# Optimization experiments

Measured on AMD Instinct MI355X. Metric: run time of the kernel, lower is better.

## Reference

```python
import jax, jax.numpy as jnp
import numpy as np

# ---- constants matching the torch module / entmax normmax_bisect defaults ----
ALPHA = 5.0                 # normmax alpha (entmax normmax_bisect default)
N_BISECT = 50               # bisection iterations
K_EXP = 1.0 / (ALPHA - 1.0)        # p_i propto (z_i - tau)_+^{1/(alpha-1)}
AK_EXP = ALPHA / (ALPHA - 1.0)     # norm condition: sum (z-tau)_+^{alpha/(alpha-1)} = 1
EPS = 1e-8                  # module epsilon
LN_EPS = 1e-5               # torch LayerNorm default eps

B, N, C, D = 32, 1024, 64, 768


def _bisect_tau(z):
    # z: [..., S]; find tau with f(tau) = sum_i relu(z_i - tau)^AK_EXP - 1 = 0 (f decreasing)
    max_val = jnp.max(z, axis=-1, keepdims=True)
    lo, hi = max_val - 1.0, max_val  # f(lo) >= 0, f(hi) = -1 < 0

    def body(_, carry):
        lo, hi = carry
        tau = 0.5 * (lo + hi)
        f = jnp.sum(jnp.maximum(z - tau, 0.0) ** AK_EXP, axis=-1, keepdims=True) - 1.0
        lo = jnp.where(f >= 0, tau, lo)
        hi = jnp.where(f >= 0, hi, tau)
        return (lo, hi)

    lo, hi = jax.lax.fori_loop(0, N_BISECT, body, (lo, hi))
    return 0.5 * (lo + hi)


def normmax_last(z):
    # normmax over last axis: p = s / sum(s), s = relu(z - tau)^{1/(alpha-1)}, ||s||_alpha = 1
    tau = _bisect_tau(z)
    u = jnp.maximum(z - tau, 0.0)
    u_safe = jnp.where(u > 0, u, 1.0)
    s = jnp.where(u > 0, u_safe ** K_EXP, 0.0)
    return s / jnp.sum(s, axis=-1, keepdims=True)


def layernorm(x, scale, bias):
    mu = jnp.mean(x, axis=-1, keepdims=True)
    var = jnp.mean((x - mu) ** 2, axis=-1, keepdims=True)
    return (x - mu) * jax.lax.rsqrt(var + LN_EPS) * scale + bias


def setup_inputs() -> dict:
    key = jax.random.key(0)
    ks = jax.random.split(key, 10)
    w = lambda k, shp: (jax.random.normal(k, shp, dtype=jnp.float32) * 0.02)
    return {
        "features": jax.random.normal(ks[0], (B, N, D), dtype=jnp.float32),
        "slots_init": jax.random.normal(ks[1], (B, C, D), dtype=jnp.float32),
        "mask": jax.random.randint(ks[2], (B, N), 0, 2, dtype=jnp.int32),
        "ln_f_scale": jnp.ones((D,), jnp.float32),
        "ln_f_bias": jnp.zeros((D,), jnp.float32),
        "ln_s_scale": jnp.ones((D,), jnp.float32),
        "ln_s_bias": jnp.zeros((D,), jnp.float32),
        "Wk": w(ks[3], (D, D)),
        "Wv": w(ks[4], (D, D)),
        "Wq": w(ks[5], (D, D)),
        "W_ih": w(ks[6], (3 * D, D)),
        "W_hh": w(ks[7], (3 * D, D)),
        "b_ih": jnp.zeros((3 * D,), jnp.float32),
        "b_hh": jnp.zeros((3 * D,), jnp.float32),
    }


def reference(features, slots_init, mask, ln_f_scale, ln_f_bias, ln_s_scale, ln_s_bias,
              Wk, Wv, Wq, W_ih, W_hh, b_ih, b_hh):
    f = layernorm(features, ln_f_scale, ln_f_bias)        # [B,N,D]
    k = f @ Wk.T
    v = f @ Wv.T
    b, n, d = v.shape
    c = slots_init.shape[1]
    m = mask[:, None, :] != 0                             # [B,1,N], broadcasts over C

    # num_iterations = 1; straight-through (detach trick) is the identity here.
    slots_prev = slots_init
    s = layernorm(slots_init, ln_s_scale, ln_s_bias)
    q = s @ Wq.T                                          # [B,C,D]
    logits = jnp.einsum('bcd,bnd->bcn', q, k) * (1.0 / np.sqrt(d))
    logits = jnp.where(m, logits, 0.0)                    # masked_fill(mask==0, 0)
    # normmax over the slot axis (dim=1)
    attn = jnp.moveaxis(normmax_last(jnp.moveaxis(logits, 1, -1)), -1, 1)  # [B,C,N]
    attn = jnp.where(m, attn, 0.0)
    attn_wm = attn / (jnp.sum(attn, axis=-1, keepdims=True) + EPS)
    updates = jnp.einsum('bcn,bnd->bcd', attn_wm, v)      # [B,C,D]

    # torch GRUCell: r,z,n gate order
    x = updates.reshape(-1, d)
    h = slots_prev.reshape(-1, d)
    gi = x @ W_ih.T + b_ih
    gh = h @ W_hh.T + b_hh
    ir, iz, in_ = jnp.split(gi, 3, axis=-1)
    hr, hz, hn = jnp.split(gh, 3, axis=-1)
    r = jax.nn.sigmoid(ir + hr)
    zg = jax.nn.sigmoid(iz + hz)
    ng = jnp.tanh(in_ + r * hn)
    h_new = (1.0 - zg) * ng + zg * h
    slots = h_new.reshape(b, c, d)
    return slots, attn
```

## Files before the change

### kernel.cpp

```cpp
#include <hip/hip_runtime.h>
#include <cstdint>
#include <cmath>

#define DEVINL __device__ __forceinline__


using f32x4  = __attribute__((ext_vector_type(4))) float;
using bf16x8 = __attribute__((ext_vector_type(8))) __bf16;
using u16x8  = __attribute__((ext_vector_type(8))) unsigned short;
using u16x4  = __attribute__((ext_vector_type(4))) unsigned short;
using fl4    = __attribute__((ext_vector_type(4))) float;

DEVINL float bf2f(unsigned short h) {
    unsigned int u = ((unsigned int)h) << 16;
    float f; __builtin_memcpy(&f, &u, 4); return f;
}
DEVINL unsigned short f2bf(float f) {
    unsigned int u; __builtin_memcpy(&u, &f, 4);
    u += 0x7FFFu + ((u >> 16) & 1u);
    return (unsigned short)(u >> 16);
}
DEVINL float sqrt_raw(float x) {
    float r; asm("v_sqrt_f32 %0, %1" : "=v"(r) : "v"(x)); return r;
}

DEVINL void gload_lds16(const unsigned short* g, unsigned short* l) {
    __builtin_amdgcn_global_load_lds(
        (__attribute__((address_space(1))) void*)g,
        (__attribute__((address_space(3))) void*)l,
        16, 0, 0);
}

__global__ __launch_bounds__(256)
void tr2_f2b_split(const float* __restrict__ Wq, const float* __restrict__ Wk,
                   unsigned short* __restrict__ WqT_i, unsigned short* __restrict__ WkT_i)
{
    constexpr int S = 768 * 768;
    const int o = blockIdx.x * 256 + threadIdx.x;
    if (o >= 2 * S) return;
    const float* x; unsigned short* y; int i;
    if (o < S) { x = Wq; y = WqT_i; i = o; }
    else       { x = Wk; y = WkT_i; i = o - S; }
    const int e = i / 768, d = i - e * 768;
    const float v = x[d * 768 + e];
    const unsigned short h = f2bf(v);
    y[(long)e * 1536 + d]       = h;
    y[(long)e * 1536 + 768 + d] = f2bf(v - bf2f(h));
}

__global__ __launch_bounds__(256)
void conv2_fused(const float* __restrict__ Wih, const float* __restrict__ Whh,
                 const float* __restrict__ sl,  const float* __restrict__ Wv,
                 unsigned short* __restrict__ Wihb, unsigned short* __restrict__ Whhb,
                 unsigned short* __restrict__ slb,  unsigned short* __restrict__ Wvb)
{
    constexpr int S1 = 3 * 768 * 768;
    constexpr int S2 = S1 + 3 * 768 * 768;
    constexpr int S3 = S2 + 32 * 64 * 768;
    constexpr int S4 = S3 + 768 * 768;
    const int i = (blockIdx.x * 256 + threadIdx.x) * 4;
    if (i >= S4) return;
    const float* src; unsigned short* dst; int off;
    if (i < S1)      { src = Wih; dst = Wihb; off = i; }
    else if (i < S2) { src = Whh; dst = Whhb; off = i - S1; }
    else if (i < S3) { src = sl;  dst = slb;  off = i - S2; }
    else             { src = Wv;  dst = Wvb;  off = i - S3; }
    fl4 v = *(const fl4*)(src + off);
    u16x4 o;
#pragma unroll
    for (int j = 0; j < 4; ++j) o[j] = f2bf(v[j]);
    *(u16x4*)(dst + off) = o;
}

template<int BM, int BN, int WAVES_M, int WAVES_N, int OUTMODE>
__global__ __launch_bounds__(256)
void gemm_bt3(const unsigned short* __restrict__ AB, const unsigned short* __restrict__ BB,
              void* __restrict__ out1,
              int N, int K, long sA, long sB, long sC, float alpha)
{
    constexpr int BK = 32;
    constexpr int WM = BM / WAVES_M, WN = BN / WAVES_N;
    constexpr int MT = WM / 16, NT = WN / 16;
    __shared__ alignas(16) unsigned short Ash[BM * BK], Asl[BM * BK];
    __shared__ alignas(16) unsigned short Bsh[BN * BK], Bsl[BN * BK];

    const int bz = blockIdx.z;
    AB += (long)bz * sA;
    BB += (long)bz * sB;
    const int row0 = blockIdx.y * BM, col0 = blockIdx.x * BN;
    const int tid = threadIdx.x, l = tid & 63, w = tid >> 6;
    const int wm = w / WAVES_N, wn = w % WAVES_N;
    const int fr = l & 15, fq = l >> 4;

    f32x4 acc[MT][NT] = {};
    constexpr int ACALLS = (BM * BK) / (256 * 8);
    constexpr int BCALLS = (BN * BK) / (256 * 8);

    for (int kt = 0; kt < K; kt += BK) {
#pragma unroll
        for (int c = 0; c < ACALLS; ++c) {
            const int e = (c * 256 + tid) * 8;
            const long rb = (long)(row0 + (e >> 5)) * (2 * K) + kt + (e & 31);
            gload_lds16(AB + rb, &Ash[e]);
            gload_lds16(AB + rb + K, &Asl[e]);
        }
#pragma unroll
        for (int c = 0; c < BCALLS; ++c) {
            const int e = (c * 256 + tid) * 8;
            const long rb = (long)(col0 + (e >> 5)) * (2 * K) + kt + (e & 31);
            gload_lds16(BB + rb, &Bsh[e]);
            gload_lds16(BB + rb + K, &Bsl[e]);
        }
        __syncthreads();

        bf16x8 afh[MT], afl[MT], bfh[NT], bfl[NT];
#pragma unroll
        for (int m = 0; m < MT; ++m) {
            const int o = (wm * WM + m * 16 + fr) * BK + fq * 8;
            afh[m] = __builtin_bit_cast(bf16x8, *(const u16x8*)&Ash[o]);
            afl[m] = __builtin_bit_cast(bf16x8, *(const u16x8*)&Asl[o]);
        }
#pragma unroll
        for (int n = 0; n < NT; ++n) {
            const int o = (wn * WN + n * 16 + fr) * BK + fq * 8;
            bfh[n] = __builtin_bit_cast(bf16x8, *(const u16x8*)&Bsh[o]);
            bfl[n] = __builtin_bit_cast(bf16x8, *(const u16x8*)&Bsl[o]);
        }
#pragma unroll
        for (int m = 0; m < MT; ++m)
#pragma unroll
            for (int n = 0; n < NT; ++n) {
                acc[m][n] = __builtin_amdgcn_mfma_f32_16x16x32_bf16(afh[m], bfh[n], acc[m][n], 0, 0, 0);
                acc[m][n] = __builtin_amdgcn_mfma_f32_16x16x32_bf16(afh[m], bfl[n], acc[m][n], 0, 0, 0);
                acc[m][n] = __builtin_amdgcn_mfma_f32_16x16x32_bf16(afl[m], bfh[n], acc[m][n], 0, 0, 0);
            }
        __syncthreads();
    }

#pragma unroll
    for (int m = 0; m < MT; ++m) {
        const int gr = row0 + wm * WM + m * 16 + fq * 4;
#pragma unroll
        for (int n = 0; n < NT; ++n) {
            const int gc = col0 + wn * WN + n * 16 + fr;
#pragma unroll
            for (int j = 0; j < 4; ++j) {
                const float v = acc[m][n][j] * alpha;
                if (OUTMODE == 0) {
                    ((float*)out1)[(long)bz * sC + (long)(gr + j) * N + gc] = v;
                } else {
                    unsigned short* ob = (unsigned short*)out1;
                    const long rb = (long)(gr + j) * (2 * N) + gc;
                    const unsigned short h = f2bf(v);
                    ob[rb] = h;
                    ob[rb + N] = f2bf(v - bf2f(h));
                }
            }
        }
    }
}

template<int BM, int BN, int WAVES_M, int WAVES_N, bool OUT_F32>
__global__ __launch_bounds__(256)
void gemm_bt(const unsigned short* __restrict__ A,
             const unsigned short* __restrict__ B,
             void* __restrict__ Cv,
             int N, int K, long sA, long sB, long sC, float alpha)
{
    constexpr int BK = 32;
    constexpr int WM = BM / WAVES_M, WN = BN / WAVES_N;
    constexpr int MT = WM / 16, NT = WN / 16;
    __shared__ alignas(16) unsigned short As[BM * BK];
    __shared__ alignas(16) unsigned short Bs[BN * BK];

    const int bz = blockIdx.z;
    A += (long)bz * sA;
    B += (long)bz * sB;
    const int row0 = blockIdx.y * BM, col0 = blockIdx.x * BN;
    const int tid = threadIdx.x, l = tid & 63, w = tid >> 6;
    const int wm = w / WAVES_N, wn = w % WAVES_N;
    const int fr = l & 15, fq = l >> 4;

    f32x4 acc[MT][NT] = {};
    constexpr int ACALLS = (BM * BK) / (256 * 8);
    constexpr int BCALLS = (BN * BK) / (256 * 8);

    for (int kt = 0; kt < K; kt += BK) {
#pragma unroll
        for (int c = 0; c < ACALLS; ++c) {
            const int e = (c * 256 + tid) * 8;
            gload_lds16(A + (long)(row0 + (e >> 5)) * K + kt + (e & 31), &As[e]);
        }
#pragma unroll
        for (int c = 0; c < BCALLS; ++c) {
            const int e = (c * 256 + tid) * 8;
            gload_lds16(B + (long)(col0 + (e >> 5)) * K + kt + (e & 31), &Bs[e]);
        }
        __syncthreads();

        bf16x8 af[MT], bfr[NT];
#pragma unroll
        for (int m = 0; m < MT; ++m)
            af[m] = __builtin_bit_cast(bf16x8, *(const u16x8*)&As[(wm * WM + m * 16 + fr) * BK + fq * 8]);
#pragma unroll
        for (int n = 0; n < NT; ++n)
            bfr[n] = __builtin_bit_cast(bf16x8, *(const u16x8*)&Bs[(wn * WN + n * 16 + fr) * BK + fq * 8]);
#pragma unroll
        for (int m = 0; m < MT; ++m)
#pragma unroll
            for (int n = 0; n < NT; ++n)
                acc[m][n] = __builtin_amdgcn_mfma_f32_16x16x32_bf16(af[m], bfr[n], acc[m][n], 0, 0, 0);
        __syncthreads();
    }

#pragma unroll
    for (int m = 0; m < MT; ++m) {
        const int gr = row0 + wm * WM + m * 16 + fq * 4;
#pragma unroll
        for (int n = 0; n < NT; ++n) {
            const int gc = col0 + wn * WN + n * 16 + fr;
#pragma unroll
            for (int j = 0; j < 4; ++j) {
                const float v = acc[m][n][j] * alpha;
                if (OUT_F32) ((float*)Cv)[(long)bz * sC + (long)(gr + j) * N + gc] = v;
                else ((unsigned short*)Cv)[(long)bz * sC + (long)(gr + j) * N + gc] = f2bf(v);
            }
        }
    }
}

template<int BM, int BN, int WAVES_M, int WAVES_N>
__global__ __launch_bounds__(256)
void gemm_nt_rs(const unsigned short* __restrict__ A,
                const unsigned short* __restrict__ Bm,
                unsigned short* __restrict__ C,
                int N, int K, long sA, long sB, long sC)
{
    constexpr int BK = 32;
    constexpr int WM = BM / WAVES_M, WN = BN / WAVES_N;
    constexpr int MT = WM / 16, NT = WN / 16;
    __shared__ alignas(16) unsigned short As[BM * BK];
    __shared__ alignas(16) unsigned short Bs[BN * BK];
    __shared__ float rsums[BM];

    const int bz = blockIdx.z;
    A += (long)bz * sA;
    Bm += (long)bz * sB;
    const int row0 = blockIdx.y * BM, col0 = blockIdx.x * BN;
    const int tid = threadIdx.x, l = tid & 63, w = tid >> 6;
    const int wm = w / WAVES_N, wn = w % WAVES_N;
    const int fr = l & 15, fq = l >> 4;

    f32x4 acc[MT][NT] = {};
    float rsum = 0.f;
    constexpr int ACALLS = (BM * BK) / (256 * 8);
    constexpr int TPR = BN / 8;
    constexpr int RPP = 256 / TPR;
    const int br = tid / TPR, bc8 = (tid % TPR) * 8;

    for (int kt = 0; kt < K; kt += BK) {
#pragma unroll
        for (int c = 0; c < ACALLS; ++c) {
            const int e = (c * 256 + tid) * 8;
            gload_lds16(A + (long)(row0 + (e >> 5)) * K + kt + (e & 31), &As[e]);
        }
#pragma unroll
        for (int p = 0; p < BK / RPP; ++p) {
            const int r = p * RPP + br;
            u16x8 vv = *(const u16x8*)(Bm + (long)(kt + r) * (2 * N) + col0 + bc8);
#pragma unroll
            for (int j = 0; j < 8; ++j) Bs[(bc8 + j) * BK + r] = vv[j];
        }
        __syncthreads();

        if (tid < BM) {
#pragma unroll
            for (int kk = 0; kk < BK / 8; ++kk) {
                u16x8 vv = *(const u16x8*)&As[tid * BK + kk * 8];
#pragma unroll
                for (int j = 0; j < 8; ++j) rsum += bf2f(vv[j]);
            }
        }

        bf16x8 af[MT], bfr[NT];
#pragma unroll
        for (int m = 0; m < MT; ++m)
            af[m] = __builtin_bit_cast(bf16x8, *(const u16x8*)&As[(wm * WM + m * 16 + fr) * BK + fq * 8]);
#pragma unroll
        for (int n = 0; n < NT; ++n)
            bfr[n] = __builtin_bit_cast(bf16x8, *(const u16x8*)&Bs[(wn * WN + n * 16 + fr) * BK + fq * 8]);
#pragma unroll
        for (int m = 0; m < MT; ++m)
#pragma unroll
            for (int n = 0; n < NT; ++n)
                acc[m][n] = __builtin_amdgcn_mfma_f32_16x16x32_bf16(af[m], bfr[n], acc[m][n], 0, 0, 0);
        __syncthreads();
    }

    if (tid < BM) rsums[tid] = rsum;
    __syncthreads();

#pragma unroll
    for (int m = 0; m < MT; ++m) {
        const int lr = wm * WM + m * 16 + fq * 4;
        const int gr = row0 + lr;
#pragma unroll
        for (int n = 0; n < NT; ++n) {
            const int gc = col0 + wn * WN + n * 16 + fr;
#pragma unroll
            for (int j = 0; j < 4; ++j) {
                const float inv = 1.f / (rsums[lr + j] + 1e-8f);
                C[(long)bz * sC + (long)(gr + j) * N + gc] = f2bf(acc[m][n][j] * inv);
            }
        }
    }
}

__global__ __launch_bounds__(256)
void ln_fused(const float* __restrict__ xf, const float* __restrict__ gf,
              const float* __restrict__ bf,
              unsigned short* __restrict__ fi,
              const float* __restrict__ xs, const float* __restrict__ gs,
              const float* __restrict__ bs,
              unsigned short* __restrict__ si,
              int nrows_f)
{
    constexpr int D = 768;
    const int lane = threadIdx.x & 63;
    long row = (long)blockIdx.x * 4 + (threadIdx.x >> 6);
    const float *x, *g, *bb_;
    unsigned short* y;
    if (row < nrows_f) { x = xf; g = gf; bb_ = bf; y = fi; }
    else { row -= nrows_f; x = xs; g = gs; bb_ = bs; y = si; }

    const float* xr = x + row * D;
    const int eA = lane * 8;
    const int eB = 512 + lane * 8;
    float v[16];
    {
        fl4 a = *(const fl4*)(xr + eA);
        fl4 b = *(const fl4*)(xr + eA + 4);
#pragma unroll
        for (int j = 0; j < 4; ++j) { v[j] = a[j]; v[4 + j] = b[j]; }
    }
    if (lane < 32) {
        fl4 a = *(const fl4*)(xr + eB);
        fl4 b = *(const fl4*)(xr + eB + 4);
#pragma unroll
        for (int j = 0; j < 4; ++j) { v[8 + j] = a[j]; v[12 + j] = b[j]; }
    }
    float s = 0.f, s2 = 0.f;
#pragma unroll
    for (int j = 0; j < 8; ++j) { s += v[j]; s2 += v[j] * v[j]; }
    if (lane < 32) {
#pragma unroll
        for (int j = 8; j < 16; ++j) { s += v[j]; s2 += v[j] * v[j]; }
    }
#pragma unroll
    for (int o = 1; o < 64; o <<= 1) { s += __shfl_xor(s, o); s2 += __shfl_xor(s2, o); }
    const float mu  = s / (float)D;
    const float var = s2 / (float)D - mu * mu;
    const float r   = rsqrtf(var + 1e-5f);

    unsigned short* yr = y + row * (2 * D);
    {
        fl4 g0 = *(const fl4*)(g + eA), g1 = *(const fl4*)(g + eA + 4);
        fl4 b0 = *(const fl4*)(bb_ + eA), b1 = *(const fl4*)(bb_ + eA + 4);
        u16x8 oh, ol;
#pragma unroll
        for (int j = 0; j < 8; ++j) {
            const float gg = (j < 4) ? g0[j] : g1[j - 4];
            const float be = (j < 4) ? b0[j] : b1[j - 4];
            const float yv = (v[j] - mu) * r * gg + be;
            oh[j] = f2bf(yv);
            ol[j] = f2bf(yv - bf2f(oh[j]));
        }
        *(u16x8*)(yr + eA) = oh;
        *(u16x8*)(yr + D + eA) = ol;
    }
    if (lane < 32) {
        fl4 g0 = *(const fl4*)(g + eB), g1 = *(const fl4*)(g + eB + 4);
        fl4 b0 = *(const fl4*)(bb_ + eB), b1 = *(const fl4*)(bb_ + eB + 4);
        u16x8 oh, ol;
#pragma unroll
        for (int j = 0; j < 8; ++j) {
            const float gg = (j < 4) ? g0[j] : g1[j - 4];
            const float be = (j < 4) ? b0[j] : b1[j - 4];
            const float yv = (v[8 + j] - mu) * r * gg + be;
            oh[j] = f2bf(yv);
            ol[j] = f2bf(yv - bf2f(oh[j]));
        }
        *(u16x8*)(yr + eB) = oh;
        *(u16x8*)(yr + D + eB) = ol;
    }
}

__global__ __launch_bounds__(256)
void normmax_cols(const float* __restrict__ logits, const int* __restrict__ mask,
                  float* __restrict__ attn_f32, unsigned short* __restrict__ attn_b16)
{
    constexpr int N = 1024, C = 64;
    const int b = blockIdx.y;
    const int tid = threadIdx.x, l = tid & 63, w = tid >> 6;
    const int n = blockIdx.x * 64 + w * 16 + (l & 15);
    const int cb = (l >> 4) * 16;
    const long base = (long)b * C * N + n;
    const float* Lb = logits + base;
    const int m = mask[b * N + n];

    float z[16];
#pragma unroll
    for (int i = 0; i < 16; ++i) z[i] = m ? Lb[(cb + i) * N] : 0.f;

    float mx = z[0];
#pragma unroll
    for (int i = 1; i < 16; ++i) mx = fmaxf(mx, z[i]);
    mx = fmaxf(mx, __shfl_xor(mx, 16));
    mx = fmaxf(mx, __shfl_xor(mx, 32));

    float lo = mx - 1.f, hi = mx;
    for (int it = 0; it < 34; ++it) {
        const float tau = 0.5f * (lo + hi);
        float f = 0.f;
#pragma unroll
        for (int i = 0; i < 16; ++i) {
            const float u = fmaxf(z[i] - tau, 0.f);
            f += u * sqrt_raw(sqrt_raw(u));
        }
        f += __shfl_xor(f, 16);
        f += __shfl_xor(f, 32);
        if (f >= 1.f) lo = tau; else hi = tau;
    }
    const float tau = 0.5f * (lo + hi);
    float sv[16]; float ss = 0.f;
#pragma unroll
    for (int i = 0; i < 16; ++i) {
        const float u = fmaxf(z[i] - tau, 0.f);
        sv[i] = sqrt_raw(sqrt_raw(u));
        ss += sv[i];
    }
    ss += __shfl_xor(ss, 16);
    ss += __shfl_xor(ss, 32);
    const float inv = 1.f / ss;
#pragma unroll
    for (int i = 0; i < 16; ++i) {
        const float a = m ? sv[i] * inv : 0.f;
        attn_f32[base + (long)(cb + i) * N] = a;
        attn_b16[base + (long)(cb + i) * N] = f2bf(a);
    }
}

__global__ __launch_bounds__(256)
void gru_gates(const float* __restrict__ gi, const float* __restrict__ gh,
               const float* __restrict__ b_ih, const float* __restrict__ b_hh,
               const float* __restrict__ h, float* __restrict__ out)
{
    constexpr int D = 768;
    const int t = blockIdx.x * 256 + threadIdx.x;
    const int row = t / (D / 4), d = (t - row * (D / 4)) * 4;
    const float* gir = gi + (long)row * 3 * D;
    const float* ghr = gh + (long)row * 3 * D;
    fl4 ir  = *(const fl4*)(gir + d);
    fl4 iz  = *(const fl4*)(gir + D + d);
    fl4 in_ = *(const fl4*)(gir + 2 * D + d);
    fl4 hr  = *(const fl4*)(ghr + d);
    fl4 hz  = *(const fl4*)(ghr + D + d);
    fl4 hn  = *(const fl4*)(ghr + 2 * D + d);
    fl4 bir = *(const fl4*)(b_ih + d);
    fl4 biz = *(const fl4*)(b_ih + D + d);
    fl4 bin = *(const fl4*)(b_ih + 2 * D + d);
    fl4 bhr = *(const fl4*)(b_hh + d);
    fl4 bhz = *(const fl4*)(b_hh + D + d);
    fl4 bhn = *(const fl4*)(b_hh + 2 * D + d);
    fl4 hv  = *(const fl4*)(h + (long)row * D + d);
    fl4 o;
#pragma unroll
    for (int j = 0; j < 4; ++j) {
        const float r  = 1.f / (1.f + expf(-(ir[j] + bir[j] + hr[j] + bhr[j])));
        const float zg = 1.f / (1.f + expf(-(iz[j] + biz[j] + hz[j] + bhz[j])));
        const float ng = tanhf(in_[j] + bin[j] + r * (hn[j] + bhn[j]));
        o[j] = (1.f - zg) * ng + zg * hv[j];
    }
    *(fl4*)(out + (long)row * D + d) = o;
}

extern "C" void kernel_launch(void* const* d_in, const int* in_sizes, int n_in,
                              void* d_out, int out_size, void* d_ws, size_t ws_size,
                              hipStream_t stream)
{
    const float* features = (const float*)d_in[0];
    const float* slots    = (const float*)d_in[1];
    const int*   mask     = (const int*)d_in[2];
    const float* lnf_g = (const float*)d_in[3];
    const float* lnf_b = (const float*)d_in[4];
    const float* lns_g = (const float*)d_in[5];
    const float* lns_b = (const float*)d_in[6];
    const float* Wk  = (const float*)d_in[7];
    const float* Wv  = (const float*)d_in[8];
    const float* Wq  = (const float*)d_in[9];
    const float* Wih = (const float*)d_in[10];
    const float* Whh = (const float*)d_in[11];
    const float* bih = (const float*)d_in[12];
    const float* bhh = (const float*)d_in[13];

    constexpr int B = 32, N = 1024, C = 64, D = 768;
    char* ws = (char*)d_ws;
    unsigned short* f_i  = (unsigned short*)(ws + 0);
    float*          gi   = (float*)(ws + 0);
    float*          gh   = (float*)(ws + 18874368);
    unsigned short* Wihb = (unsigned short*)(ws + 37748736);
    unsigned short* Whhb = (unsigned short*)(ws + 41287680);
    unsigned short* Wvb  = (unsigned short*)(ws + 44826624);
    unsigned short* updb = (unsigned short*)(ws + 57671680);
    unsigned short* slb  = (unsigned short*)(ws + 60817408);
    float*          lg     = (float*)(ws + 100663296);
    unsigned short* s_i    = (unsigned short*)(ws + 109051904);
    unsigned short* ab16   = (unsigned short*)(ws + 109051904);
    unsigned short* qk_i   = (unsigned short*)(ws + 115343360);
    unsigned short* Pbf    = (unsigned short*)(ws + 115343360);
    unsigned short* WqT_i  = (unsigned short*)(ws + 121634816);
    unsigned short* WkT_i  = (unsigned short*)(ws + 123994112);
    unsigned short* M_i    = (unsigned short*)(ws + 126353408);

    float* out_slots = (float*)d_out;
    float* out_attn  = out_slots + (long)B * C * D;

    tr2_f2b_split<<<(2 * D * D + 255) / 256, 256, 0, stream>>>(Wq, Wk, WqT_i, WkT_i);

    ln_fused<<<(B * N + B * C) / 4, 256, 0, stream>>>(
        features, lnf_g, lnf_b, f_i,
        slots, lns_g, lns_b, s_i, B * N);

    gemm_bt3<64, 64, 2, 2, 1><<<dim3(D / 64, D / 64, 1), 256, 0, stream>>>(
        WkT_i, WqT_i, M_i, D, D, 0, 0, 0, 1.f);
    gemm_bt3<64, 64, 2, 2, 1><<<dim3(D / 64, (B * C) / 64, 1), 256, 0, stream>>>(
        s_i, M_i, qk_i, D, D, 0, 0, 0, 1.f);
    gemm_bt3<64, 64, 2, 2, 0><<<dim3(N / 64, 1, B), 256, 0, stream>>>(
        qk_i, f_i, lg,
        N, D, (long)C * 2 * D, (long)N * 2 * D, (long)C * N, 0.03608439182435161f);

    normmax_cols<<<dim3(N / 64, B), 256, 0, stream>>>(lg, mask, out_attn, ab16);

    gemm_nt_rs<64, 64, 2, 2><<<dim3(D / 64, 1, B), 256, 0, stream>>>(
        ab16, f_i, Pbf, D, N, (long)C * N, (long)N * 2 * D, (long)C * D);

    {
        constexpr int TOT = 3 * D * D + 3 * D * D + B * C * D + D * D;
        conv2_fused<<<(TOT / 4 + 255) / 256, 256, 0, stream>>>(
            Wih, Whh, slots, Wv, Wihb, Whhb, slb, Wvb);
    }

    gemm_bt<64, 64, 2, 2, false><<<dim3(D / 64, (B * C) / 64, 1), 256, 0, stream>>>(
        Pbf, Wvb, updb, D, D, 0, 0, 0, 1.f);

    gemm_bt<128, 128, 2, 2, true><<<dim3(3 * D / 128, (B * C) / 128, 2), 256, 0, stream>>>(
        updb, Wihb, gi, 3 * D, D,
        (long)(B * C) * D, (long)(3 * D) * D, (long)(B * C) * 3 * D, 1.f);

    gru_gates<<<(B * C * D / 4) / 256, 256, 0, stream>>>(gi, gh, bih, bhh, slots, out_slots);
}
```

Measured before the change: 227.1 us.

## Compact unmasked tokens per batch and skip masked work across pipeline

Adds a per-batch mask scan that builds a compacted index list of valid tokens plus a count and a count padded to a multiple of 64. LayerNorm on features, the logits GEMM, normmax and the attention-weighted GEMM then work only on the compacted rows. Tiles past the padded count exit early, and the gathered attention is scattered back to the original token positions. Masked tokens contribute exactly zero, so this removes roughly the masked fraction of memory traffic and compute. In exchange it adds a scan kernel and a full zero-fill of the attention output, and the reads become indirect gathers.

```diff
diff --git a/kernel.cpp b/kernel.cpp
--- a/kernel.cpp
+++ b/kernel.cpp
@@ -29,6 +29,44 @@
         (__attribute__((address_space(1))) void*)g,
         (__attribute__((address_space(3))) void*)l,
         16, 0, 0);
+}
+
+__global__ __launch_bounds__(256)
+void mask_scan(const int* __restrict__ mask, int* __restrict__ idx,
+               int* __restrict__ cnt, int* __restrict__ cpad)
+{
+    constexpr int NB = 1024;
+    const int b = blockIdx.x * 4 + (threadIdx.x >> 6);
+    const int lane = threadIdx.x & 63;
+    if (b >= 32) return;
+    const int* mrow = mask + b * NB;
+    int loc[16]; int lsum = 0;
+#pragma unroll
+    for (int i = 0; i < 16; ++i) { loc[i] = mrow[lane * 16 + i] != 0; lsum += loc[i]; }
+    int pre = lsum;
+#pragma unroll
+    for (int o = 1; o < 64; o <<= 1) {
+        int t = __shfl_up(pre, o);
+        if (lane >= o) pre += t;
+    }
+    const int total = __shfl(pre, 63);
+    pre -= lsum;
+    int* ib = idx + b * NB;
+    int p = pre;
+#pragma unroll
+    for (int i = 0; i < 16; ++i) if (loc[i]) ib[p++] = lane * 16 + i;
+    if (lane == 0) {
+        cnt[b] = total;
+        int cp = (total + 63) & ~63;
+        cpad[b] = cp < 64 ? 64 : cp;
+    }
+}
+
+__global__ __launch_bounds__(256)
+void zfill(float* __restrict__ p, int n4)
+{
+    const int i = blockIdx.x * 256 + threadIdx.x;
+    if (i < n4) { fl4 z = {0.f, 0.f, 0.f, 0.f}; *(fl4*)(p + i * 4) = z; }
 }
 
 __global__ __launch_bounds__(256)
@@ -75,7 +113,7 @@
 template<int BM, int BN, int WAVES_M, int WAVES_N, int OUTMODE>
 __global__ __launch_bounds__(256)
 void gemm_bt3(const unsigned short* __restrict__ AB, const unsigned short* __restrict__ BB,
-              void* __restrict__ out1,
+              void* __restrict__ out1, const int* __restrict__ cpad,
               int N, int K, long sA, long sB, long sC, float alpha)
 {
     constexpr int BK = 32;
@@ -85,9 +123,10 @@
     __shared__ alignas(16) unsigned short Bsh[BN * BK], Bsl[BN * BK];
 
     const int bz = blockIdx.z;
+    const int row0 = blockIdx.y * BM, col0 = blockIdx.x * BN;
+    if (cpad && col0 >= cpad[bz]) return;
     AB += (long)bz * sA;
     BB += (long)bz * sB;
-    const int row0 = blockIdx.y * BM, col0 = blockIdx.x * BN;
     const int tid = threadIdx.x, l = tid & 63, w = tid >> 6;
     const int wm = w / WAVES_N, wn = w % WAVES_N;
     const int fr = l & 15, fq = l >> 4;
@@ -234,7 +273,8 @@
 void gemm_nt_rs(const unsigned short* __restrict__ A,
                 const unsigned short* __restrict__ Bm,
                 unsigned short* __restrict__ C,
-                int N, int K, long sA, long sB, long sC)
+                const int* __restrict__ cpad,
+                int N, int Kmax, long sA, long sB, long sC)
 {
     constexpr int BK = 32;
     constexpr int WM = BM / WAVES_M, WN = BN / WAVES_N;
@@ -244,6 +284,7 @@
     __shared__ float rsums[BM];
 
     const int bz = blockIdx.z;
+    const int Keff = cpad[bz];
     A += (long)bz * sA;
     Bm += (long)bz * sB;
     const int row0 = blockIdx.y * BM, col0 = blockIdx.x * BN;
@@ -258,11 +299,11 @@
     constexpr int RPP = 256 / TPR;
     const int br = tid / TPR, bc8 = (tid % TPR) * 8;
 
-    for (int kt = 0; kt < K; kt += BK) {
+    for (int kt = 0; kt < Keff; kt += BK) {
 #pragma unroll
         for (int c = 0; c < ACALLS; ++c) {
             const int e = (c * 256 + tid) * 8;
-            gload_lds16(A + (long)(row0 + (e >> 5)) * K + kt + (e & 31), &As[e]);
+            gload_lds16(A + (long)(row0 + (e >> 5)) * Kmax + kt + (e & 31), &As[e]);
         }
 #pragma unroll
         for (int p = 0; p < BK / RPP; ++p) {
@@ -317,35 +358,53 @@
 }
 
 __global__ __launch_bounds__(256)
-void ln_fused(const float* __restrict__ xf, const float* __restrict__ gf,
-              const float* __restrict__ bf,
-              unsigned short* __restrict__ fi,
-              const float* __restrict__ xs, const float* __restrict__ gs,
-              const float* __restrict__ bs,
-              unsigned short* __restrict__ si,
-              int nrows_f)
+void ln_fused_c(const float* __restrict__ xf, const float* __restrict__ gf,
+                const float* __restrict__ bf,
+                unsigned short* __restrict__ fi,
+                const float* __restrict__ xs, const float* __restrict__ gs,
+                const float* __restrict__ bs,
+                unsigned short* __restrict__ si,
+                const int* __restrict__ idx, const int* __restrict__ cnt,
+                const int* __restrict__ cpad, int nrows_f)
 {
     constexpr int D = 768;
     const int lane = threadIdx.x & 63;
     long row = (long)blockIdx.x * 4 + (threadIdx.x >> 6);
     const float *x, *g, *bb_;
     unsigned short* y;
-    if (row < nrows_f) { x = xf; g = gf; bb_ = bf; y = fi; }
-    else { row -= nrows_f; x = xs; g = gs; bb_ = bs; y = si; }
-
-    const float* xr = x + row * D;
+    long srow;
+    if (row < nrows_f) {
+        const int b = (int)(row >> 10), j = (int)(row & 1023);
+        if (j >= cpad[b]) return;
+        y = fi; srow = row;
+        unsigned short* yr = y + srow * (2 * D);
+        if (j >= cnt[b]) {
+            u16x8 z = {};
+            unsigned short* p = yr + lane * 24;
+            *(u16x8*)p = z; *(u16x8*)(p + 8) = z; *(u16x8*)(p + 16) = z;
+            return;
+        }
+        const int n = idx[(b << 10) + j];
+        x = xf + ((long)(b << 10) + n) * D;
+        g = gf; bb_ = bf;
+    } else {
+        srow = row - nrows_f;
+        x = xs + srow * D;
+        g = gs; bb_ = bs; y = si;
+    }
+
     const int eA = lane * 8;
     const int eB = 512 + lane * 8;
     float v[16];
     {
-        fl4 a = *(const fl4*)(xr + eA);
-        fl4 b = *(const fl4*)(xr + eA + 4);
+        fl4 a = *(const fl4*)(x + eA);
+        fl4 b = *(const fl4*)(x + eA + 4);
 #pragma unroll
         for (int j = 0; j < 4; ++j) { v[j] = a[j]; v[4 + j] = b[j]; }
     }
     if (lane < 32) {
-        fl4 a = *(const fl4*)(xr + eB);
-        fl4 b = *(const fl4*)(xr + eB + 4);
+        fl4 a = *(const fl4*)(x + eB);
+        fl4 b = *(const fl4*)(x + eB + 4);
 #pragma unroll
         for (int j = 0; j < 4; ++j) { v[8 + j] = a[j]; v[12 + j] = b[j]; }
     }
@@ -362,7 +421,7 @@
     const float var = s2 / (float)D - mu * mu;
     const float r   = rsqrtf(var + 1e-5f);
 
-    unsigned short* yr = y + row * (2 * D);
+    unsigned short* yr = (row < nrows_f ? fi : si) + srow * (2 * D);
     {
         fl4 g0 = *(const fl4*)(g + eA), g1 = *(const fl4*)(g + eA + 4);
         fl4 b0 = *(const fl4*)(bb_ + eA), b1 = *(const fl4*)(bb_ + eA + 4);
@@ -396,21 +455,24 @@
 }
 
 __global__ __launch_bounds__(256)
-void normmax_cols(const float* __restrict__ logits, const int* __restrict__ mask,
-                  float* __restrict__ attn_f32, unsigned short* __restrict__ attn_b16)
+void normmax_cols_c(const float* __restrict__ logits,
+                    const int* __restrict__ idx, const int* __restrict__ cnt,
+                    const int* __restrict__ cpad,
+                    float* __restrict__ attn_f32, unsigned short* __restrict__ attn_b16)
 {
     constexpr int N = 1024, C = 64;
     const int b = blockIdx.y;
+    const int j0 = blockIdx.x * 64;
+    if (j0 >= cpad[b]) return;
     const int tid = threadIdx.x, l = tid & 63, w = tid >> 6;
-    const int n = blockIdx.x * 64 + w * 16 + (l & 15);
+    const int j = j0 + w * 16 + (l & 15);
     const int cb = (l >> 4) * 16;
-    const long base = (long)b * C * N + n;
-    const float* Lb = logits + base;
-    const int m = mask[b * N + n];
+    const long base = (long)b * C * N + j;
+    const bool valid = j < cnt[b];
 
     float z[16];
 #pragma unroll
-    for (int i = 0; i < 16; ++i) z[i] = m ? Lb[(cb + i) * N] : 0.f;
+    for (int i = 0; i < 16; ++i) z[i] = valid ? logits[base + (long)(cb + i) * N] : 0.f;
 
     float mx = z[0];
 #pragma unroll
@@ -442,11 +504,12 @@
     ss += __shfl_xor(ss, 16);
     ss += __shfl_xor(ss, 32);
     const float inv = 1.f / ss;
+    const int n = valid ? idx[(b << 10) + j] : 0;
 #pragma unroll
     for (int i = 0; i < 16; ++i) {
-        const float a = m ? sv[i] * inv : 0.f;
-        attn_f32[base + (long)(cb + i) * N] = a;
+        const float a = valid ? sv[i] * inv : 0.f;
         attn_b16[base + (long)(cb + i) * N] = f2bf(a);
+        if (valid) attn_f32[(long)b * C * N + (long)(cb + i) * N + n] = a;
     }
 }
 
@@ -521,28 +584,35 @@
     unsigned short* WqT_i  = (unsigned short*)(ws + 121634816);
     unsigned short* WkT_i  = (unsigned short*)(ws + 123994112);
     unsigned short* M_i    = (unsigned short*)(ws + 126353408);
+    int*            idx    = (int*)(ws + 128712704);
+    int*            cnt    = (int*)(ws + 128843776);
+    int*            cpad   = (int*)(ws + 128843904);
 
     float* out_slots = (float*)d_out;
     float* out_attn  = out_slots + (long)B * C * D;
 
+    mask_scan<<<8, 256, 0, stream>>>(mask, idx, cnt, cpad);
+    zfill<<<(B * C * N / 4 + 255) / 256, 256, 0, stream>>>(out_attn, B * C * N / 4);
+
     tr2_f2b_split<<<(2 * D * D + 255) / 256, 256, 0, stream>>>(Wq, Wk, WqT_i, WkT_i);
 
-    ln_fused<<<(B * N + B * C) / 4, 256, 0, stream>>>(
+    ln_fused_c<<<(B * N + B * C) / 4, 256, 0, stream>>>(
         features, lnf_g, lnf_b, f_i,
-        slots, lns_g, lns_b, s_i, B * N);
+        slots, lns_g, lns_b, s_i,
+        idx, cnt, cpad, B * N);
 
     gemm_bt3<64, 64, 2, 2, 1><<<dim3(D / 64, D / 64, 1), 256, 0, stream>>>(
-        WkT_i, WqT_i, M_i, D, D, 0, 0, 0, 1.f);
+        WkT_i, WqT_i, M_i, nullptr, D, D, 0, 0, 0, 1.f);
     gemm_bt3<64, 64, 2, 2, 1><<<dim3(D / 64, (B * C) / 64, 1), 256, 0, stream>>>(
-        s_i, M_i, qk_i, D, D, 0, 0, 0, 1.f);
+        s_i, M_i, qk_i, nullptr, D, D, 0, 0, 0, 1.f);
     gemm_bt3<64, 64, 2, 2, 0><<<dim3(N / 64, 1, B), 256, 0, stream>>>(
-        qk_i, f_i, lg,
+        qk_i, f_i, lg, cpad,
         N, D, (long)C * 2 * D, (long)N * 2 * D, (long)C * N, 0.03608439182435161f);
 
-    normmax_cols<<<dim3(N / 64, B), 256, 0, stream>>>(lg, mask, out_attn, ab16);
+    normmax_cols_c<<<dim3(N / 64, B), 256, 0, stream>>>(lg, idx, cnt, cpad, out_attn, ab16);
 
     gemm_nt_rs<64, 64, 2, 2><<<dim3(D / 64, 1, B), 256, 0, stream>>>(
-        ab16, f_i, Pbf, D, N, (long)C * N, (long)N * 2 * D, (long)C * D);
+        ab16, f_i, Pbf, cpad, D, N, (long)C * N, (long)N * 2 * D, (long)C * D);
 
     {
         constexpr int TOT = 3 * D * D + 3 * D * D + B * C * D + D * D;
```

After: 202.4 us. 1.12x faster.
